# Optimization experiments

Hardware: AMD Instinct MI355X
Metric: run time of the kernel (lower is better)

Reference implementation:

```python
import jax, jax.numpy as jnp
import numpy as np

DIMS = [2048, 2048, 2048, 2048, 1000]
BATCH = 1024
N_RELAX = 25
RELAX_LR = 0.3
N_LAYERS = len(DIMS) - 1  # 4 weight matrices, states indexed 0..4


def setup_inputs() -> dict:
    key = jax.random.key(0)
    ks = jax.random.split(key, N_LAYERS + 1)
    inp = {"x": jax.random.normal(ks[0], (BATCH, DIMS[0]), jnp.float32)}
    for i in range(N_LAYERS):
        scale = np.float32(np.sqrt(2.0 / DIMS[i]))
        inp[f"W{i}"] = jax.random.normal(ks[i + 1], (DIMS[i], DIMS[i + 1]), jnp.float32) * scale
    # biases[0] is never used in forward; biases[1..4] init to zeros as in torch code
    for l in range(1, N_LAYERS + 1):
        inp[f"b{l}"] = jnp.zeros((DIMS[l],), jnp.float32)
    return inp


def _rho(t):
    return jnp.clip(t, 0.0, 1.0)


def _relax(x, Ws, bs):
    # bs[l-1] corresponds to original biases[l] (state l's bias), l = 1..N_LAYERS
    # feedforward initialization pass
    states = [x]
    h = x
    for l in range(N_LAYERS):
        h = _rho(h @ Ws[l] + bs[l])
        states.append(h)

    # Gauss-Seidel sweep: states[l-1] already updated this iteration when l uses it
    def sweep(carry, _):
        full = [x] + list(carry)
        for l in range(1, N_LAYERS + 1):
            ds = -full[l] + bs[l - 1] + _rho(full[l - 1]) @ Ws[l - 1]
            if l < N_LAYERS:
                ds = ds + _rho(full[l + 1]) @ Ws[l].T
            full[l] = _rho(full[l] + RELAX_LR * ds)
        return tuple(full[1:]), None

    carry, _ = jax.lax.scan(sweep, tuple(states[1:]), None, length=N_RELAX)
    return carry


def reference(x, W0, W1, W2, W3, b1, b2, b3, b4):
    Ws = [W0, W1, W2, W3]
    bs = [b1, b2, b3, b4]
    states = _relax(x, Ws, bs)
    return states[-1]  # [BATCH, DIMS[-1]]
```

## Files before the change

kernel.cpp:

```cpp
#include <hip/hip_runtime.h>

typedef _Float16 fp16_t;
typedef _Float16 v8h __attribute__((ext_vector_type(8)));
typedef float    v4f __attribute__((ext_vector_type(4)));

#define RELAX_LR 0.3f

__device__ __forceinline__ void async_cp16(const void* g, void* l) {
    __builtin_amdgcn_global_load_lds(
        (const __attribute__((address_space(1))) void*)g,
        (__attribute__((address_space(3))) void*)l, 16, 0, 0);
}

struct GJob {
    const fp16_t *A1, *B1t, *A2, *B2t;
    fp16_t* part;
    int K1, K2s, CK, Ntot;
};

__global__ __launch_bounds__(256, 4) void gemm_splitk_kernel(GJob j0, GJob j1, int nb0)
{
    __shared__ __align__(16) fp16_t As[2][128][32];
    __shared__ __align__(16) fp16_t Bs[2][128][32];

    const int tid  = threadIdx.x;
    const int lane = tid & 63;
    const int w    = tid >> 6;
    const int wm   = w >> 1;
    const int wn   = w & 1;
    const int quad = lane >> 4;
    const int lrow = lane & 15;

    int bblk = blockIdx.x;
    const GJob j = (bblk < nb0) ? j0 : j1;
    if (bblk >= nb0) bblk -= nb0;

    const int low3 = bblk & 7;
    const int g    = bblk >> 3;
    const int bm   = g & 7;
    const int c    = (g >> 3) * 8 + low3;
    const int bn   = c >> 3;
    const int z    = c & 7;
    const int k0   = z * j.CK;

    const int sr = lane >> 2;
    const int sc = (lane & 3) * 8;
    const size_t rowA = (size_t)(bm * 128 + 32 * w + sr);
    const size_t rowB = (size_t)(bn * 128 + 32 * w + sr);
    const fp16_t* a1 = j.A1  + rowA * j.K1 + sc;
    const fp16_t* b1 = j.B1t + rowB * j.K1 + sc;
    const fp16_t* a2 = j.A2  ? j.A2  + rowA * j.K2s + sc : nullptr;
    const fp16_t* b2 = j.B2t ? j.B2t + rowB * j.K2s + sc : nullptr;
    const size_t s16a = (size_t)16 * j.K1;
    const size_t s16b = (size_t)16 * j.K2s;

    auto stage = [&](int buf, int kc) {
        const fp16_t *a0, *b0; size_t st;
        if (kc < j.K1) { a0 = a1 + kc;          b0 = b1 + kc;          st = s16a; }
        else           { a0 = a2 + (kc - j.K1); b0 = b2 + (kc - j.K1); st = s16b; }
        async_cp16(a0,      &As[buf][32 * w     ][0]);
        async_cp16(a0 + st, &As[buf][32 * w + 16][0]);
        async_cp16(b0,      &Bs[buf][32 * w     ][0]);
        async_cp16(b0 + st, &Bs[buf][32 * w + 16][0]);
    };

    v4f acc[4][4] = {};
    const int iters = j.CK >> 5;

    stage(0, k0);

    for (int it = 0; it < iters; ++it) {
        __syncthreads();
        if (it + 1 < iters) stage((it + 1) & 1, k0 + (it + 1) * 32);
        const int cur = it & 1;
        v8h af[4], bv[4];
        #pragma unroll
        for (int fm = 0; fm < 4; ++fm)
            af[fm] = *(const v8h*)&As[cur][wm * 64 + fm * 16 + lrow][quad * 8];
        #pragma unroll
        for (int fn = 0; fn < 4; ++fn)
            bv[fn] = *(const v8h*)&Bs[cur][wn * 64 + fn * 16 + lrow][quad * 8];
        #pragma unroll
        for (int fm = 0; fm < 4; ++fm)
            #pragma unroll
            for (int fn = 0; fn < 4; ++fn)
                acc[fm][fn] = __builtin_amdgcn_mfma_f32_16x16x32_f16(
                    af[fm], bv[fn], acc[fm][fn], 0, 0, 0);
    }

    fp16_t* po = j.part + (size_t)z * 1024 * j.Ntot;
    const int rowbase = bm * 128 + wm * 64 + quad * 4;
    const int colbase = bn * 128 + wn * 64;
    #pragma unroll
    for (int fn = 0; fn < 4; ++fn) {
        const int col = colbase + fn * 16 + lrow;
        #pragma unroll
        for (int fm = 0; fm < 4; ++fm) {
            const int row = rowbase + fm * 16;
            #pragma unroll
            for (int r = 0; r < 4; ++r)
                po[(size_t)(row + r) * j.Ntot + col] = (fp16_t)acc[fm][fn][r];
        }
    }
}

struct RJob {
    const fp16_t* part;
    const float* bias;
    const float* extra;
    const fp16_t* s_old;
    fp16_t* outb;
    float* finout;
    int nz, Ntot, do_update;
};

__global__ __launch_bounds__(256) void reduce_update_kernel(RJob j0, RJob j1, int nb0)
{
    int b = blockIdx.x;
    const RJob j = (b < nb0) ? j0 : j1;
    if (b >= nb0) b -= nb0;
    const size_t e = ((size_t)b * 256 + threadIdx.x) * 8;

    float v[8];
    {
        const v8h p0 = *(const v8h*)(j.part + e);
        #pragma unroll
        for (int k = 0; k < 8; ++k) v[k] = (float)p0[k];
    }
    for (int z = 1; z < j.nz; ++z) {
        const v8h p = *(const v8h*)(j.part + (size_t)z * 1024 * j.Ntot + e);
        #pragma unroll
        for (int k = 0; k < 8; ++k) v[k] += (float)p[k];
    }
    const int col = (int)e & (j.Ntot - 1);
    if (j.extra) {
        const float4 e0 = *(const float4*)(j.extra + e);
        const float4 e1 = *(const float4*)(j.extra + e + 4);
        v[0] += e0.x; v[1] += e0.y; v[2] += e0.z; v[3] += e0.w;
        v[4] += e1.x; v[5] += e1.y; v[6] += e1.z; v[7] += e1.w;
    } else {
        const float4 b0 = *(const float4*)(j.bias + col);
        const float4 b1 = *(const float4*)(j.bias + col + 4);
        v[0] += b0.x; v[1] += b0.y; v[2] += b0.z; v[3] += b0.w;
        v[4] += b1.x; v[5] += b1.y; v[6] += b1.z; v[7] += b1.w;
    }
    if (j.do_update) {
        const v8h so = *(const v8h*)(j.s_old + e);
        #pragma unroll
        for (int k = 0; k < 8; ++k) {
            const float s = (float)so[k];
            v[k] = s + RELAX_LR * (v[k] - s);
        }
    }
    #pragma unroll
    for (int k = 0; k < 8; ++k) v[k] = fminf(fmaxf(v[k], 0.f), 1.f);
    v8h h;
    #pragma unroll
    for (int k = 0; k < 8; ++k) h[k] = (fp16_t)v[k];
    *(v8h*)(j.outb + e) = h;

    if (j.finout && col < 1000) {
        const int row = (int)(e >> 10);
        float* o = j.finout + (size_t)row * 1000 + col;
        float4 o0 = {v[0], v[1], v[2], v[3]};
        float4 o1 = {v[4], v[5], v[6], v[7]};
        *(float4*)o       = o0;
        *(float4*)(o + 4) = o1;
    }
}

__global__ __launch_bounds__(256) void makec1_kernel(
    const fp16_t* __restrict__ part, const float* __restrict__ bias,
    float* __restrict__ c1f, int total8)
{
    const int i = blockIdx.x * 256 + threadIdx.x;
    if (i >= total8) return;
    const size_t e = (size_t)i * 8;
    float v[8];
    {
        const v8h p0 = *(const v8h*)(part + e);
        #pragma unroll
        for (int k = 0; k < 8; ++k) v[k] = (float)p0[k];
    }
    #pragma unroll
    for (int z = 1; z < 8; ++z) {
        const v8h p = *(const v8h*)(part + (size_t)z * 1024 * 2048 + e);
        #pragma unroll
        for (int k = 0; k < 8; ++k) v[k] += (float)p[k];
    }
    const int col = (int)e & 2047;
    const float4 b0 = *(const float4*)(bias + col);
    const float4 b1 = *(const float4*)(bias + col + 4);
    v[0] += b0.x; v[1] += b0.y; v[2] += b0.z; v[3] += b0.w;
    v[4] += b1.x; v[5] += b1.y; v[6] += b1.z; v[7] += b1.w;
    float4 o0 = {v[0], v[1], v[2], v[3]};
    float4 o1 = {v[4], v[5], v[6], v[7]};
    *(float4*)(c1f + e)     = o0;
    *(float4*)(c1f + e + 4) = o1;
}

__global__ void conv_w_kernel(const float* __restrict__ W, int R, int C,
                              fp16_t* Wb, fp16_t* __restrict__ WbT,
                              int Rp, int Cp)
{
    __shared__ float t[32][33];
    const int tx = threadIdx.x & 31;
    const int ty = threadIdx.x >> 5;
    const int r0 = blockIdx.y * 32;
    const int c0 = blockIdx.x * 32;
    #pragma unroll
    for (int i = 0; i < 4; ++i) {
        const int r = r0 + ty + i * 8;
        const int c = c0 + tx;
        float v = 0.f;
        if (r < R && c < C) v = W[(size_t)r * C + c];
        t[ty + i * 8][tx] = v;
    }
    __syncthreads();
    if (Wb) {
        #pragma unroll
        for (int i = 0; i < 4; ++i) {
            const int r = r0 + ty + i * 8;
            const int c = c0 + tx;
            if (r < Rp && c < Cp) Wb[(size_t)r * Cp + c] = (fp16_t)t[ty + i * 8][tx];
        }
    }
    #pragma unroll
    for (int i = 0; i < 4; ++i) {
        const int cc = c0 + ty + i * 8;
        const int rr = r0 + tx;
        if (cc < Cp && rr < Rp) WbT[(size_t)cc * Rp + rr] = (fp16_t)t[tx][ty + i * 8];
    }
}

__global__ void conv_x_kernel(const float* __restrict__ x,
                              fp16_t* __restrict__ xb, fp16_t* __restrict__ rxb, int n)
{
    const int i = blockIdx.x * blockDim.x + threadIdx.x;
    if (i < n) {
        const float v = x[i];
        xb[i]  = (fp16_t)v;
        rxb[i] = (fp16_t)fminf(fmaxf(v, 0.f), 1.f);
    }
}

__global__ void pad_b4_kernel(const float* __restrict__ b4, float* __restrict__ b4p)
{
    const int i = blockIdx.x * blockDim.x + threadIdx.x;
    if (i < 1024) b4p[i] = (i < 1000) ? b4[i] : 0.f;
}

extern "C" void kernel_launch(void* const* d_in, const int* in_sizes, int n_in,
                              void* d_out, int out_size, void* d_ws, size_t ws_size,
                              hipStream_t stream)
{
    const float* x  = (const float*)d_in[0];
    const float* W0 = (const float*)d_in[1];
    const float* W1 = (const float*)d_in[2];
    const float* W2 = (const float*)d_in[3];
    const float* W3 = (const float*)d_in[4];
    const float* b1 = (const float*)d_in[5];
    const float* b2 = (const float*)d_in[6];
    const float* b3 = (const float*)d_in[7];
    const float* b4 = (const float*)d_in[8];
    float* out = (float*)d_out;

    char* p = (char*)d_ws;
    auto alloc = [&](size_t bytes) {
        char* q = p;
        p += (bytes + 255) & ~(size_t)255;
        return q;
    };

    fp16_t* xb    = (fp16_t*)alloc((size_t)1024 * 2048 * 2);
    fp16_t* rxb   = (fp16_t*)alloc((size_t)1024 * 2048 * 2);
    fp16_t* Wb1   = (fp16_t*)alloc((size_t)2048 * 2048 * 2);
    fp16_t* Wb2   = (fp16_t*)alloc((size_t)2048 * 2048 * 2);
    fp16_t* Wb3   = (fp16_t*)alloc((size_t)2048 * 1024 * 2);
    fp16_t* WbT0  = (fp16_t*)alloc((size_t)2048 * 2048 * 2);
    fp16_t* WbT1  = (fp16_t*)alloc((size_t)2048 * 2048 * 2);
    fp16_t* WbT2  = (fp16_t*)alloc((size_t)2048 * 2048 * 2);
    fp16_t* WbT3  = (fp16_t*)alloc((size_t)1024 * 2048 * 2);
    fp16_t* s1b   = (fp16_t*)alloc((size_t)1024 * 2048 * 2);
    fp16_t* s2b   = (fp16_t*)alloc((size_t)1024 * 2048 * 2);
    fp16_t* s3b   = (fp16_t*)alloc((size_t)1024 * 2048 * 2);
    fp16_t* s4b   = (fp16_t*)alloc((size_t)1024 * 1024 * 2);
    float*  b4p   = (float*)alloc(1024 * 4);
    float*  c1f   = (float*)alloc((size_t)1024 * 2048 * 4);
    fp16_t* partA = (fp16_t*)alloc((size_t)8 * 1024 * 1024 * 2);
    fp16_t* partB = (fp16_t*)alloc((size_t)8 * 1024 * 2048 * 2);
    (void)ws_size; (void)in_sizes; (void)n_in; (void)out_size;

    conv_x_kernel<<<(1024 * 2048 + 255) / 256, 256, 0, stream>>>(x, xb, rxb, 1024 * 2048);
    pad_b4_kernel<<<4, 256, 0, stream>>>(b4, b4p);
    conv_w_kernel<<<dim3(64, 64), 256, 0, stream>>>(W0, 2048, 2048, nullptr, WbT0, 2048, 2048);
    conv_w_kernel<<<dim3(64, 64), 256, 0, stream>>>(W1, 2048, 2048, Wb1, WbT1, 2048, 2048);
    conv_w_kernel<<<dim3(64, 64), 256, 0, stream>>>(W2, 2048, 2048, Wb2, WbT2, 2048, 2048);
    conv_w_kernel<<<dim3(32, 64), 256, 0, stream>>>(W3, 2048, 1000, Wb3, WbT3, 2048, 1024);

    const dim3 blk(256);
    const int rg2048 = 1024 * 2048 / 8 / 256;
    const int rg1024 = 1024 * 1024 / 8 / 256;

    const GJob jC1 = { rxb, WbT0, nullptr, nullptr, partB, 2048, 0,    256, 2048 };
    const GJob jI1 = { xb,  WbT0, nullptr, nullptr, partB, 2048, 0,    256, 2048 };
    const GJob jI2 = { s1b, WbT1, nullptr, nullptr, partB, 2048, 0,    256, 2048 };
    const GJob jI3 = { s2b, WbT2, nullptr, nullptr, partB, 2048, 0,    256, 2048 };
    const GJob jI4 = { s3b, WbT3, nullptr, nullptr, partA, 2048, 0,    256, 1024 };
    const GJob jL1 = { s2b, Wb1,  nullptr, nullptr, partB, 2048, 0,    256, 2048 };
    const GJob jL2 = { s1b, WbT1, s3b, Wb2,         partB, 2048, 2048, 512, 2048 };
    const GJob jL3 = { s2b, WbT2, s4b, Wb3,         partB, 2048, 1024, 384, 2048 };
    const GJob jL4 = { s3b, WbT3, nullptr, nullptr, partA, 2048, 0,    256, 1024 };

    const RJob rI1 = { partB, b1,  nullptr, nullptr, s1b, nullptr, 8, 2048, 0 };
    const RJob rI2 = { partB, b2,  nullptr, nullptr, s2b, nullptr, 8, 2048, 0 };
    const RJob rI3 = { partB, b3,  nullptr, nullptr, s3b, nullptr, 8, 2048, 0 };
    const RJob rI4 = { partA, b4p, nullptr, nullptr, s4b, nullptr, 8, 1024, 0 };
    const RJob rL1 = { partB, nullptr, c1f, s1b, s1b, nullptr, 8, 2048, 1 };
    const RJob rL2 = { partB, b2,  nullptr, s2b, s2b, nullptr, 8, 2048, 1 };
    const RJob rL3 = { partB, b3,  nullptr, s3b, s3b, nullptr, 8, 2048, 1 };
    const RJob rL4 = { partA, b4p, nullptr, s4b, s4b, nullptr, 8, 1024, 1 };
    RJob rL4f = rL4; rL4f.finout = out;

    gemm_splitk_kernel<<<1024, blk, 0, stream>>>(jC1, jC1, 1024);
    makec1_kernel<<<rg2048, blk, 0, stream>>>(partB, b1, c1f, 1024 * 2048 / 8);

    gemm_splitk_kernel<<<1024, blk, 0, stream>>>(jI1, jI1, 1024);
    reduce_update_kernel<<<rg2048, blk, 0, stream>>>(rI1, rI1, rg2048);
    gemm_splitk_kernel<<<1024, blk, 0, stream>>>(jI2, jI2, 1024);
    reduce_update_kernel<<<rg2048, blk, 0, stream>>>(rI2, rI2, rg2048);
    gemm_splitk_kernel<<<1024, blk, 0, stream>>>(jI3, jI3, 1024);
    reduce_update_kernel<<<rg2048, blk, 0, stream>>>(rI3, rI3, rg2048);
    gemm_splitk_kernel<<<512, blk, 0, stream>>>(jI4, jI4, 512);
    reduce_update_kernel<<<rg1024, blk, 0, stream>>>(rI4, rI4, rg1024);

    gemm_splitk_kernel<<<1024, blk, 0, stream>>>(jL1, jL1, 1024);
    reduce_update_kernel<<<rg2048, blk, 0, stream>>>(rL1, rL1, rg2048);
    for (int it = 0; it < 25; ++it) {
        gemm_splitk_kernel<<<1024, blk, 0, stream>>>(jL2, jL2, 1024);
        reduce_update_kernel<<<rg2048, blk, 0, stream>>>(rL2, rL2, rg2048);
        gemm_splitk_kernel<<<1024, blk, 0, stream>>>(jL3, jL3, 1024);
        reduce_update_kernel<<<rg2048, blk, 0, stream>>>(rL3, rL3, rg2048);
        if (it < 24) {
            gemm_splitk_kernel<<<1536, blk, 0, stream>>>(jL4, jL1, 512);
            reduce_update_kernel<<<rg1024 + rg2048, blk, 0, stream>>>(rL4, rL1, rg1024);
        } else {
            gemm_splitk_kernel<<<512, blk, 0, stream>>>(jL4, jL4, 512);
            reduce_update_kernel<<<rg1024, blk, 0, stream>>>(rL4f, rL4f, rg1024);
        }
    }
}
```

Before: 2.650 ms.

## Enlarge split-K GEMM tiles to 256x256 with triple-buffered swizzled LDS pipeline

Rewrites the split-K GEMM to use 512-thread blocks computing 256x256 output tiles, with a 3-stage LDS ring buffer, XOR-swizzled LDS layout, split A/B staging interleaved with MFMA phases, and setprio around compute. The intent is more data reuse per loaded tile, fewer LDS bank conflicts, and better overlap of global loads with MFMA work. Grid sizes drop by 4x (256 or 128 blocks per GEMM), which may underfill the GPU's many CUs and raises register pressure from 32 accumulators per thread.

```diff
diff --git a/kernel.cpp b/kernel.cpp
--- a/kernel.cpp
+++ b/kernel.cpp
@@ -18,16 +18,15 @@
     int K1, K2s, CK, Ntot;
 };
 
-__global__ __launch_bounds__(256, 4) void gemm_splitk_kernel(GJob j0, GJob j1, int nb0)
-{
-    __shared__ __align__(16) fp16_t As[2][128][32];
-    __shared__ __align__(16) fp16_t Bs[2][128][32];
+__global__ __launch_bounds__(512, 2) void gemm_splitk_kernel(GJob j0, GJob j1, int nb0)
+{
+    __shared__ __align__(16) fp16_t smem[3][2][256][32];
 
     const int tid  = threadIdx.x;
     const int lane = tid & 63;
     const int w    = tid >> 6;
-    const int wm   = w >> 1;
-    const int wn   = w & 1;
+    const int wr   = w >> 2;
+    const int wc   = w & 3;
     const int quad = lane >> 4;
     const int lrow = lane & 15;
 
@@ -35,71 +34,108 @@
     const GJob j = (bblk < nb0) ? j0 : j1;
     if (bblk >= nb0) bblk -= nb0;
 
-    const int low3 = bblk & 7;
-    const int g    = bblk >> 3;
-    const int bm   = g & 7;
-    const int c    = (g >> 3) * 8 + low3;
-    const int bn   = c >> 3;
-    const int z    = c & 7;
-    const int k0   = z * j.CK;
-
-    const int sr = lane >> 2;
-    const int sc = (lane & 3) * 8;
-    const size_t rowA = (size_t)(bm * 128 + 32 * w + sr);
-    const size_t rowB = (size_t)(bn * 128 + 32 * w + sr);
-    const fp16_t* a1 = j.A1  + rowA * j.K1 + sc;
-    const fp16_t* b1 = j.B1t + rowB * j.K1 + sc;
-    const fp16_t* a2 = j.A2  ? j.A2  + rowA * j.K2s + sc : nullptr;
-    const fp16_t* b2 = j.B2t ? j.B2t + rowB * j.K2s + sc : nullptr;
-    const size_t s16a = (size_t)16 * j.K1;
-    const size_t s16b = (size_t)16 * j.K2s;
-
-    auto stage = [&](int buf, int kc) {
-        const fp16_t *a0, *b0; size_t st;
-        if (kc < j.K1) { a0 = a1 + kc;          b0 = b1 + kc;          st = s16a; }
-        else           { a0 = a2 + (kc - j.K1); b0 = b2 + (kc - j.K1); st = s16b; }
-        async_cp16(a0,      &As[buf][32 * w     ][0]);
-        async_cp16(a0 + st, &As[buf][32 * w + 16][0]);
-        async_cp16(b0,      &Bs[buf][32 * w     ][0]);
-        async_cp16(b0 + st, &Bs[buf][32 * w + 16][0]);
+    const int xcd = bblk & 7;
+    const int idx = bblk >> 3;
+    int bm, bn;
+    if (j.Ntot == 2048) { bm = idx >> 3; bn = idx & 7; }
+    else                { bm = idx >> 2; bn = idx & 3; }
+    const int z  = xcd;
+    const int k0 = z * j.CK;
+    const int nt = j.CK >> 5;
+
+    const int srow = lane >> 2;
+    const int swz  = ((lane & 3) ^ (srow & 3)) * 8;
+    const int arow = bm * 256 + w * 16 + srow;
+    const int brow = bn * 256 + w * 16 + srow;
+    const fp16_t* a1 = j.A1  + (size_t)arow * j.K1 + swz;
+    const fp16_t* b1 = j.B1t + (size_t)brow * j.K1 + swz;
+    const fp16_t* a2 = j.A2  ? j.A2  + (size_t)arow * j.K2s + swz : nullptr;
+    const fp16_t* b2 = j.B2t ? j.B2t + (size_t)brow * j.K2s + swz : nullptr;
+
+    auto stageA = [&](int buf, int kc) {
+        const fp16_t* s; size_t st;
+        if (kc < j.K1) { s = a1 + kc;          st = (size_t)128 * j.K1;  }
+        else           { s = a2 + (kc - j.K1); st = (size_t)128 * j.K2s; }
+        async_cp16(s,      &smem[buf][0][w * 16][0]);
+        async_cp16(s + st, &smem[buf][0][128 + w * 16][0]);
     };
-
-    v4f acc[4][4] = {};
-    const int iters = j.CK >> 5;
-
-    stage(0, k0);
-
-    for (int it = 0; it < iters; ++it) {
-        __syncthreads();
-        if (it + 1 < iters) stage((it + 1) & 1, k0 + (it + 1) * 32);
-        const int cur = it & 1;
-        v8h af[4], bv[4];
+    auto stageB = [&](int buf, int kc) {
+        const fp16_t* s; size_t st;
+        if (kc < j.K1) { s = b1 + kc;          st = (size_t)128 * j.K1;  }
+        else           { s = b2 + (kc - j.K1); st = (size_t)128 * j.K2s; }
+        async_cp16(s,      &smem[buf][1][w * 16][0]);
+        async_cp16(s + st, &smem[buf][1][128 + w * 16][0]);
+    };
+
+    v4f acc[8][4] = {};
+
+    stageA(0, k0);          stageB(0, k0);
+    stageA(1, k0 + 32);     stageB(1, k0 + 32);
+    asm volatile("s_waitcnt vmcnt(4)" ::: "memory");
+    __builtin_amdgcn_s_barrier();
+
+    int cur = 0;
+    for (int t = 0; t < nt; ++t) {
+        const int nx2 = (cur + 2 >= 3) ? cur - 1 : cur + 2;
+        const bool pf = (t + 2 < nt);
+        v8h Af[4], Bf[4];
+
+        if (pf) stageA(nx2, k0 + (t + 2) * 32);
         #pragma unroll
         for (int fm = 0; fm < 4; ++fm)
-            af[fm] = *(const v8h*)&As[cur][wm * 64 + fm * 16 + lrow][quad * 8];
+            Af[fm] = *(const v8h*)&smem[cur][0][wr * 128 + fm * 16 + lrow]
+                                        [(quad ^ (lrow & 3)) * 8];
         #pragma unroll
         for (int fn = 0; fn < 4; ++fn)
-            bv[fn] = *(const v8h*)&Bs[cur][wn * 64 + fn * 16 + lrow][quad * 8];
+            Bf[fn] = *(const v8h*)&smem[cur][1][wc * 64 + fn * 16 + lrow]
+                                        [(quad ^ (lrow & 3)) * 8];
+        __builtin_amdgcn_s_barrier();
+        asm volatile("s_waitcnt lgkmcnt(0)" ::: "memory");
+        __builtin_amdgcn_sched_barrier(0);
+        __builtin_amdgcn_s_setprio(1);
         #pragma unroll
         for (int fm = 0; fm < 4; ++fm)
             #pragma unroll
             for (int fn = 0; fn < 4; ++fn)
                 acc[fm][fn] = __builtin_amdgcn_mfma_f32_16x16x32_f16(
-                    af[fm], bv[fn], acc[fm][fn], 0, 0, 0);
+                    Af[fm], Bf[fn], acc[fm][fn], 0, 0, 0);
+        __builtin_amdgcn_s_setprio(0);
+        __builtin_amdgcn_s_barrier();
+
+        if (pf) stageB(nx2, k0 + (t + 2) * 32);
+        #pragma unroll
+        for (int fm = 0; fm < 4; ++fm)
+            Af[fm] = *(const v8h*)&smem[cur][0][wr * 128 + (4 + fm) * 16 + lrow]
+                                        [(quad ^ (lrow & 3)) * 8];
+        __builtin_amdgcn_s_barrier();
+        asm volatile("s_waitcnt lgkmcnt(0)" ::: "memory");
+        __builtin_amdgcn_sched_barrier(0);
+        __builtin_amdgcn_s_setprio(1);
+        #pragma unroll
+        for (int fm = 0; fm < 4; ++fm)
+            #pragma unroll
+            for (int fn = 0; fn < 4; ++fn)
+                acc[4 + fm][fn] = __builtin_amdgcn_mfma_f32_16x16x32_f16(
+                    Af[fm], Bf[fn], acc[4 + fm][fn], 0, 0, 0);
+        __builtin_amdgcn_s_setprio(0);
+        if (pf)                 asm volatile("s_waitcnt vmcnt(4)" ::: "memory");
+        else if (t + 1 < nt)    asm volatile("s_waitcnt vmcnt(0)" ::: "memory");
+        __builtin_amdgcn_s_barrier();
+        cur = (cur + 1 == 3) ? 0 : cur + 1;
     }
 
     fp16_t* po = j.part + (size_t)z * 1024 * j.Ntot;
-    const int rowbase = bm * 128 + wm * 64 + quad * 4;
-    const int colbase = bn * 128 + wn * 64;
+    const int rowb = bm * 256 + wr * 128 + quad * 4;
+    const int colb = bn * 256 + wc * 64 + lrow;
     #pragma unroll
     for (int fn = 0; fn < 4; ++fn) {
-        const int col = colbase + fn * 16 + lrow;
-        #pragma unroll
-        for (int fm = 0; fm < 4; ++fm) {
-            const int row = rowbase + fm * 16;
+        const int col = colb + fn * 16;
+        #pragma unroll
+        for (int fm = 0; fm < 8; ++fm) {
+            const int row0 = rowb + fm * 16;
             #pragma unroll
             for (int r = 0; r < 4; ++r)
-                po[(size_t)(row + r) * j.Ntot + col] = (fp16_t)acc[fm][fn][r];
+                po[(size_t)(row0 + r) * j.Ntot + col] = (fp16_t)acc[fm][fn][r];
         }
     }
 }
@@ -298,7 +334,8 @@
     conv_w_kernel<<<dim3(64, 64), 256, 0, stream>>>(W2, 2048, 2048, Wb2, WbT2, 2048, 2048);
     conv_w_kernel<<<dim3(32, 64), 256, 0, stream>>>(W3, 2048, 1000, Wb3, WbT3, 2048, 1024);
 
-    const dim3 blk(256);
+    const dim3 blk(512);
+    const dim3 rblk(256);
     const int rg2048 = 1024 * 2048 / 8 / 256;
     const int rg1024 = 1024 * 1024 / 8 / 256;
 
@@ -322,31 +359,31 @@
     const RJob rL4 = { partA, b4p, nullptr, s4b, s4b, nullptr, 8, 1024, 1 };
     RJob rL4f = rL4; rL4f.finout = out;
 
-    gemm_splitk_kernel<<<1024, blk, 0, stream>>>(jC1, jC1, 1024);
-    makec1_kernel<<<rg2048, blk, 0, stream>>>(partB, b1, c1f, 1024 * 2048 / 8);
-
-    gemm_splitk_kernel<<<1024, blk, 0, stream>>>(jI1, jI1, 1024);
-    reduce_update_kernel<<<rg2048, blk, 0, stream>>>(rI1, rI1, rg2048);
-    gemm_splitk_kernel<<<1024, blk, 0, stream>>>(jI2, jI2, 1024);
-    reduce_update_kernel<<<rg2048, blk, 0, stream>>>(rI2, rI2, rg2048);
-    gemm_splitk_kernel<<<1024, blk, 0, stream>>>(jI3, jI3, 1024);
-    reduce_update_kernel<<<rg2048, blk, 0, stream>>>(rI3, rI3, rg2048);
-    gemm_splitk_kernel<<<512, blk, 0, stream>>>(jI4, jI4, 512);
-    reduce_update_kernel<<<rg1024, blk, 0, stream>>>(rI4, rI4, rg1024);
-
-    gemm_splitk_kernel<<<1024, blk, 0, stream>>>(jL1, jL1, 1024);
-    reduce_update_kernel<<<rg2048, blk, 0, stream>>>(rL1, rL1, rg2048);
+    gemm_splitk_kernel<<<256, blk, 0, stream>>>(jC1, jC1, 256);
+    makec1_kernel<<<rg2048, rblk, 0, stream>>>(partB, b1, c1f, 1024 * 2048 / 8);
+
+    gemm_splitk_kernel<<<256, blk, 0, stream>>>(jI1, jI1, 256);
+    reduce_update_kernel<<<rg2048, rblk, 0, stream>>>(rI1, rI1, rg2048);
+    gemm_splitk_kernel<<<256, blk, 0, stream>>>(jI2, jI2, 256);
+    reduce_update_kernel<<<rg2048, rblk, 0, stream>>>(rI2, rI2, rg2048);
+    gemm_splitk_kernel<<<256, blk, 0, stream>>>(jI3, jI3, 256);
+    reduce_update_kernel<<<rg2048, rblk, 0, stream>>>(rI3, rI3, rg2048);
+    gemm_splitk_kernel<<<128, blk, 0, stream>>>(jI4, jI4, 128);
+    reduce_update_kernel<<<rg1024, rblk, 0, stream>>>(rI4, rI4, rg1024);
+
+    gemm_splitk_kernel<<<256, blk, 0, stream>>>(jL1, jL1, 256);
+    reduce_update_kernel<<<rg2048, rblk, 0, stream>>>(rL1, rL1, rg2048);
     for (int it = 0; it < 25; ++it) {
-        gemm_splitk_kernel<<<1024, blk, 0, stream>>>(jL2, jL2, 1024);
-        reduce_update_kernel<<<rg2048, blk, 0, stream>>>(rL2, rL2, rg2048);
-        gemm_splitk_kernel<<<1024, blk, 0, stream>>>(jL3, jL3, 1024);
-        reduce_update_kernel<<<rg2048, blk, 0, stream>>>(rL3, rL3, rg2048);
+        gemm_splitk_kernel<<<256, blk, 0, stream>>>(jL2, jL2, 256);
+        reduce_update_kernel<<<rg2048, rblk, 0, stream>>>(rL2, rL2, rg2048);
+        gemm_splitk_kernel<<<256, blk, 0, stream>>>(jL3, jL3, 256);
+        reduce_update_kernel<<<rg2048, rblk, 0, stream>>>(rL3, rL3, rg2048);
         if (it < 24) {
-            gemm_splitk_kernel<<<1536, blk, 0, stream>>>(jL4, jL1, 512);
-            reduce_update_kernel<<<rg1024 + rg2048, blk, 0, stream>>>(rL4, rL1, rg1024);
+            gemm_splitk_kernel<<<384, blk, 0, stream>>>(jL4, jL1, 128);
+            reduce_update_kernel<<<rg1024 + rg2048, rblk, 0, stream>>>(rL4, rL1, rg1024);
         } else {
-            gemm_splitk_kernel<<<512, blk, 0, stream>>>(jL4, jL4, 512);
-            reduce_update_kernel<<<rg1024, blk, 0, stream>>>(rL4f, rL4f, rg1024);
+            gemm_splitk_kernel<<<128, blk, 0, stream>>>(jL4, jL4, 128);
+            reduce_update_kernel<<<rg1024, rblk, 0, stream>>>(rL4f, rL4f, rg1024);
         }
     }
 }
```

Measured after the change: 3.003 ms. 13.3% more time.
